# Optimization experiments

Measured on AMD Instinct MI355X. Metric: run time of the kernel, lower is better.

Reference implementation:

```python
import jax, jax.numpy as jnp
import numpy as np

B, S, E, H = 8, 1024, 64, 8
DK = E // H  # n_wires per head
DIM = 2 ** DK  # statevector size


def _quantum_projection(x, phi):
    """Faithful batched simulation of _QLayer for every (batch, seq, head).
    Encoder RX(x_i) followed by trainable RX(phi_i) on the same wire equals
    RX(x_i + phi_i). Then a CNOT ring, then <Z_w> for each wire.
    x: [B,S,E] float, phi: [H,DK] float -> [B,S,E] float expectations.
    """
    b, s, e = x.shape
    theta = x.reshape(b, s, H, DK) + phi  # [B,S,H,DK]
    M = b * s * H
    th = theta.reshape(M, DK)
    # RX(t)|0> = cos(t/2)|0> - i sin(t/2)|1>
    c = jnp.cos(th * 0.5).astype(jnp.complex64)
    sn = (jnp.sin(th * 0.5) * (-1j)).astype(jnp.complex64)
    q = jnp.stack([c, sn], axis=-1)  # [M, DK, 2]
    # product state via iterated kron over the DK wires (fixed small loop)
    amps = jnp.ones((M, 1), jnp.complex64)
    for w in range(DK):
        amps = (amps[:, :, None] * q[:, w, None, :]).reshape(M, -1)
    st = amps.reshape((M,) + (2,) * DK)
    # CNOT ring: (0,1),(1,2),...,(DK-2,DK-1),(DK-1,0)
    gates = [(w, w + 1) for w in range(DK - 1)] + [(DK - 1, 0)]
    for cw, tw in gates:
        ac = 1 + cw
        s0 = jnp.take(st, 0, axis=ac)  # control = 0: identity
        s1 = jnp.take(st, 1, axis=ac)  # control = 1: flip target
        at = 1 + tw - (1 if tw > cw else 0)  # target axis after removing control axis
        s1 = jnp.flip(s1, axis=at)
        st = jnp.stack([s0, s1], axis=ac)
    stf = st.reshape(M, DIM)
    probs = stf.real ** 2 + stf.imag ** 2  # [M, DIM]
    # <Z_w> = sum_k probs[k] * (1 - 2*bit_w(k)); wire 0 is most-significant bit
    bits = (jnp.arange(DIM)[:, None] >> jnp.arange(DK - 1, -1, -1)[None, :]) & 1
    signs = (1 - 2 * bits).astype(probs.dtype)  # [DIM, DK]
    expz = probs @ signs  # [M, DK]
    return expz.reshape(b, s, e)


def setup_inputs() -> dict:
    key = jax.random.key(0)
    k1, k2, k3, k4 = jax.random.split(key, 4)
    x = jax.random.normal(k1, (B, S, E), dtype=jnp.float32)
    phi = jax.random.normal(k2, (H, DK), dtype=jnp.float32) * 0.1  # trainable RX params
    lim = 1.0 / np.sqrt(E)
    W = jax.random.uniform(k3, (E, E), jnp.float32, -lim, lim)  # combine Linear weight
    b = jax.random.uniform(k4, (E,), jnp.float32, -lim, lim)    # combine Linear bias
    return {"x": x, "phi": phi, "W": W, "b": b}


def reference(x, phi, W, b):
    # q = k = v = _projection(x): the original calls _projection(x) 3 times with
    # the same params and no randomness, so they are identical; compute once.
    proj = _quantum_projection(x, phi)  # [B,S,E]
    scores = jax.nn.softmax(
        jnp.einsum('bse,bte->bst', proj, proj) / jnp.sqrt(jnp.float32(DK)), axis=-1)
    # dropout is identity in eval mode
    ctx = jnp.einsum('bst,bte->bse', scores, proj)
    return ctx @ W.T + b
```

## Files before the change

kernel.cpp:

```cpp
#include <hip/hip_runtime.h>
#include <hip/hip_bf16.h>

#define BB 8
#define SS 1024
#define EE 64
#define HH 8
#define DKW 8

typedef __hip_bfloat16 bf16;
typedef unsigned short u16;
typedef _Float16 half8v __attribute__((ext_vector_type(8)));
typedef float floatx4 __attribute__((ext_vector_type(4)));

#define MFMA16(a, b, c) __builtin_amdgcn_mfma_f32_16x16x32_f16(a, b, c, 0, 0, 0)

#define OFF_PROJT ((size_t)BB * SS * EE * 2)

template <int NT>
__device__ __forceinline__ bool detect_f32(const u16* __restrict__ base,
                                           int tid, int* red) {
    int cnt = 0;
#pragma unroll
    for (int i = tid; i < 2048; i += NT) {
        u16 u = base[i * 2];
        int ex = (u >> 7) & 0xFF;
        cnt += (ex >= 0x84) ? 1 : 0;
    }
#pragma unroll
    for (int off = 32; off > 0; off >>= 1) cnt += __shfl_xor(cnt, off, 64);
    if ((tid & 63) == 0) red[tid >> 6] = cnt;
    __syncthreads();
    int tot = 0;
#pragma unroll
    for (int w = 0; w < NT / 64; ++w) tot += red[w];
    return tot > 64;
}

__device__ __forceinline__ void proj_compute(const void* x, const void* phi,
                                             bool f32, int m, float* z) {
    int h = m & (HH - 1);
    float th[DKW];
    if (f32) {
        const float4* xp = (const float4*)((const float*)x + (size_t)m * DKW);
        const float4* pp = (const float4*)((const float*)phi + h * DKW);
        float4 x0 = xp[0], x1 = xp[1];
        float4 p0 = pp[0], p1 = pp[1];
        th[0] = x0.x + p0.x; th[1] = x0.y + p0.y; th[2] = x0.z + p0.z; th[3] = x0.w + p0.w;
        th[4] = x1.x + p1.x; th[5] = x1.y + p1.y; th[6] = x1.z + p1.z; th[7] = x1.w + p1.w;
    } else {
        union { uint4 u; bf16 hv[8]; } xu, pu;
        xu.u = *(const uint4*)((const bf16*)x + (size_t)m * DKW);
        pu.u = *(const uint4*)((const bf16*)phi + (size_t)h * DKW);
#pragma unroll
        for (int j = 0; j < DKW; ++j)
            th[j] = __bfloat162float(xu.hv[j]) + __bfloat162float(pu.hv[j]);
    }
    float c[DKW];
#pragma unroll
    for (int j = 0; j < DKW; ++j) c[j] = __cosf(th[j]);
    float suf = c[1];
#pragma unroll
    for (int j = 2; j < DKW; ++j) suf *= c[j];
    z[0] = suf;
    float pre = c[0];
#pragma unroll
    for (int w = 1; w < DKW; ++w) { pre *= c[w]; z[w] = pre; }
}

__global__ __launch_bounds__(256) void proj_f16_kernel(const void* __restrict__ x,
                                                       const void* __restrict__ phi,
                                                       _Float16* __restrict__ projH,
                                                       _Float16* __restrict__ projT) {
    __shared__ int redd[4];
    __shared__ _Float16 zt[EE][40];
    const int tid = threadIdx.x;
    const bool f32 = detect_f32<256>((const u16*)x, tid, redd);

    const int m = blockIdx.x * 256 + tid;
    float z[DKW];
    proj_compute(x, phi, f32, m, z);

    union { half8v v; _Float16 h[8]; } o;
#pragma unroll
    for (int j = 0; j < DKW; ++j) o.h[j] = (_Float16)z[j];
    *(half8v*)(projH + (size_t)m * DKW) = o.v;

    const int h = m & (HH - 1);
    const int sl = (tid >> 3) & 31;
#pragma unroll
    for (int j = 0; j < DKW; ++j) zt[h * DKW + j][sl] = o.h[j];
    __syncthreads();

    const int b = blockIdx.x >> 5;
    const int s0 = (blockIdx.x * 32) & (SS - 1);
    const int row = tid >> 2, ch = tid & 3;
    half8v vv = *(const half8v*)(&zt[row][ch * 8]);
    *(half8v*)(projT + ((size_t)(b * EE + row)) * SS + s0 + ch * 8) = vv;
}

#define STRD 1048
__global__ __launch_bounds__(512) void fused_attn(const _Float16* __restrict__ projH,
                                                  const _Float16* __restrict__ projT,
                                                  const void* __restrict__ Wp,
                                                  const void* __restrict__ biasp,
                                                  void* __restrict__ outp) {
    __shared__ _Float16 Stile[32][STRD];
    __shared__ _Float16 ctx_lds[32][72];
    __shared__ float rowsum[32];
    __shared__ int redd[8];

    const int tid = threadIdx.x;
    const int wave = tid >> 6, lane = tid & 63;
    const int lr = lane & 15, quad = lane >> 4;
    const int b = blockIdx.y;
    const int m0 = blockIdx.x * 32;

    const bool f32 = detect_f32<512>((const u16*)Wp, tid, redd);

    const _Float16* Pb = projH + (size_t)b * SS * EE;
    const float scale = 0.35355339059327373f;

    {
        const int rowg = wave >> 2, colg = wave & 3;
        const _Float16* arow = Pb + (size_t)(m0 + rowg * 16 + lr) * EE;
        half8v a0 = *(const half8v*)(arow + quad * 8);
        half8v a1 = *(const half8v*)(arow + 32 + quad * 8);
#pragma unroll 4
        for (int c = 0; c < 16; ++c) {
            int n = colg * 256 + c * 16;
            const _Float16* brow = Pb + (size_t)(n + lr) * EE;
            half8v b0 = *(const half8v*)(brow + quad * 8);
            half8v b1 = *(const half8v*)(brow + 32 + quad * 8);
            floatx4 acc = {0.f, 0.f, 0.f, 0.f};
            acc = MFMA16(a0, b0, acc);
            acc = MFMA16(a1, b1, acc);
#pragma unroll
            for (int r = 0; r < 4; ++r)
                Stile[rowg * 16 + quad * 4 + r][n + lr] = (_Float16)(acc[r] * scale);
        }
    }
    __syncthreads();

    {
        const int row = tid >> 4, seg = tid & 15;
        half8v hv[8];
#pragma unroll
        for (int i = 0; i < 8; ++i)
            hv[i] = *(const half8v*)(&Stile[row][i * 128 + seg * 8]);
        float mloc = -1e30f;
#pragma unroll
        for (int i = 0; i < 8; ++i)
#pragma unroll
            for (int j = 0; j < 8; ++j) mloc = fmaxf(mloc, (float)hv[i][j]);
#pragma unroll
        for (int off = 1; off < 16; off <<= 1)
            mloc = fmaxf(mloc, __shfl_xor(mloc, off, 64));
        float lsum = 0.f;
#pragma unroll
        for (int i = 0; i < 8; ++i) {
#pragma unroll
            for (int j = 0; j < 8; ++j) {
                float e = __expf((float)hv[i][j] - mloc);
                lsum += e;
                hv[i][j] = (_Float16)(e * 256.f);
            }
        }
#pragma unroll
        for (int off = 1; off < 16; off <<= 1)
            lsum += __shfl_xor(lsum, off, 64);
        if (seg == 0) rowsum[row] = lsum;
#pragma unroll
        for (int i = 0; i < 8; ++i)
            *(half8v*)(&Stile[row][i * 128 + seg * 8]) = hv[i];
    }
    __syncthreads();

    {
        const int rowg = wave >> 2, cw = wave & 3;
        const _Float16* srow = &Stile[rowg * 16 + lr][0];
        const _Float16* vrow = projT + ((size_t)b * EE + cw * 16 + lr) * SS;
        floatx4 acc0 = {0.f, 0.f, 0.f, 0.f};
        floatx4 acc1 = {0.f, 0.f, 0.f, 0.f};
#pragma unroll 4
        for (int t = 0; t < SS; t += 64) {
            half8v aA = *(const half8v*)(srow + t + quad * 8);
            half8v vA = *(const half8v*)(vrow + t + quad * 8);
            half8v aB = *(const half8v*)(srow + t + 32 + quad * 8);
            half8v vB = *(const half8v*)(vrow + t + 32 + quad * 8);
            acc0 = MFMA16(aA, vA, acc0);
            acc1 = MFMA16(aB, vB, acc1);
        }
#pragma unroll
        for (int r = 0; r < 4; ++r) {
            int row_l = rowg * 16 + quad * 4 + r;
            float inv = 1.0f / (256.0f * rowsum[row_l]);
            ctx_lds[row_l][cw * 16 + lr] = (_Float16)((acc0[r] + acc1[r]) * inv);
        }
    }
    __syncthreads();

    {
        const int rowg = wave >> 2, og = wave & 3;
        const int o = og * 16 + lr;
        half8v ca0 = *(const half8v*)(&ctx_lds[rowg * 16 + lr][quad * 8]);
        half8v ca1 = *(const half8v*)(&ctx_lds[rowg * 16 + lr][32 + quad * 8]);
        half8v wb0, wb1;
        if (f32) {
            const float* wr = (const float*)Wp + (size_t)o * EE;
            union { half8v v; _Float16 h[8]; } w0, w1;
#pragma unroll
            for (int j = 0; j < 8; ++j) {
                w0.h[j] = (_Float16)wr[quad * 8 + j];
                w1.h[j] = (_Float16)wr[32 + quad * 8 + j];
            }
            wb0 = w0.v; wb1 = w1.v;
        } else {
            const bf16* wr = (const bf16*)Wp + (size_t)o * EE;
            union { uint4 u; bf16 hv[8]; } r0, r1;
            r0.u = *(const uint4*)(wr + quad * 8);
            r1.u = *(const uint4*)(wr + 32 + quad * 8);
            union { half8v v; _Float16 h[8]; } w0, w1;
#pragma unroll
            for (int j = 0; j < 8; ++j) {
                w0.h[j] = (_Float16)__bfloat162float(r0.hv[j]);
                w1.h[j] = (_Float16)__bfloat162float(r1.hv[j]);
            }
            wb0 = w0.v; wb1 = w1.v;
        }
        floatx4 oacc = {0.f, 0.f, 0.f, 0.f};
        oacc = MFMA16(ca0, wb0, oacc);
        oacc = MFMA16(ca1, wb1, oacc);

        float bo = f32 ? ((const float*)biasp)[o]
                       : __bfloat162float(((const bf16*)biasp)[o]);
#pragma unroll
        for (int r = 0; r < 4; ++r) {
            size_t oi = ((size_t)b * SS + m0 + rowg * 16 + quad * 4 + r) * EE + o;
            float val = oacc[r] + bo;
            if (f32) ((float*)outp)[oi] = val;
            else     ((bf16*)outp)[oi] = __float2bfloat16(val);
        }
    }
}

extern "C" void kernel_launch(void* const* d_in, const int* in_sizes, int n_in,
                              void* d_out, int out_size, void* d_ws, size_t ws_size,
                              hipStream_t stream) {
    const void* x    = d_in[0];
    const void* phi  = d_in[1];
    const void* W    = d_in[2];
    const void* bias = d_in[3];

    _Float16* projH = (_Float16*)d_ws;
    _Float16* projT = (_Float16*)((char*)d_ws + OFF_PROJT);

    proj_f16_kernel<<<dim3(BB * SS * HH / 256), dim3(256), 0, stream>>>(x, phi, projH, projT);
    fused_attn<<<dim3(SS / 32, BB), dim3(512), 0, stream>>>(projH, projT, W, bias, d_out);
}
```

Baseline: 85.04 us.

## Halve query tile to 16 rows, XOR-swizzle score LDS, split PV over key halves

Each block now handles 16 query rows instead of 32, so the grid doubles to 512 blocks and LDS use per block roughly halves, which allows more blocks per CU. The padded score tile is replaced by an XOR-swizzled layout to avoid LDS bank conflicts without padding. The PV product is split across two key halves handled by separate wave groups, with partial sums reduced through shared memory. The cost is an extra barrier and reduction, half the waves idle in the output projection, and keys and values are reloaded by twice as many blocks.

```diff
diff --git a/kernel.cpp b/kernel.cpp
--- a/kernel.cpp
+++ b/kernel.cpp
@@ -98,22 +98,26 @@
     *(half8v*)(projT + ((size_t)(b * EE + row)) * SS + s0 + ch * 8) = vv;
 }
 
-#define STRD 1048
+__device__ __forceinline__ int sidx(int row, int colblk) {
+    return row * 1024 + ((colblk ^ (row & 7)) << 3);
+}
+
 __global__ __launch_bounds__(512) void fused_attn(const _Float16* __restrict__ projH,
                                                   const _Float16* __restrict__ projT,
                                                   const void* __restrict__ Wp,
                                                   const void* __restrict__ biasp,
                                                   void* __restrict__ outp) {
-    __shared__ _Float16 Stile[32][STRD];
-    __shared__ _Float16 ctx_lds[32][72];
-    __shared__ float rowsum[32];
-    __shared__ int redd[8];
+    __shared__ _Float16 Stile[16 * 1024];
+    __shared__ float    pacc[4][16][17];
+    __shared__ _Float16 ctx_lds[16][72];
+    __shared__ float    rowsum[16];
+    __shared__ int      redd[8];
 
     const int tid = threadIdx.x;
     const int wave = tid >> 6, lane = tid & 63;
     const int lr = lane & 15, quad = lane >> 4;
     const int b = blockIdx.y;
-    const int m0 = blockIdx.x * 32;
+    const int m0 = blockIdx.x * 16;
 
     const bool f32 = detect_f32<512>((const u16*)Wp, tid, redd);
 
@@ -121,13 +125,12 @@
     const float scale = 0.35355339059327373f;
 
     {
-        const int rowg = wave >> 2, colg = wave & 3;
-        const _Float16* arow = Pb + (size_t)(m0 + rowg * 16 + lr) * EE;
+        const _Float16* arow = Pb + (size_t)(m0 + lr) * EE;
         half8v a0 = *(const half8v*)(arow + quad * 8);
         half8v a1 = *(const half8v*)(arow + 32 + quad * 8);
 #pragma unroll 4
-        for (int c = 0; c < 16; ++c) {
-            int n = colg * 256 + c * 16;
+        for (int c = 0; c < 8; ++c) {
+            int n = wave * 128 + c * 16;
             const _Float16* brow = Pb + (size_t)(n + lr) * EE;
             half8v b0 = *(const half8v*)(brow + quad * 8);
             half8v b1 = *(const half8v*)(brow + 32 + quad * 8);
@@ -135,29 +138,31 @@
             acc = MFMA16(a0, b0, acc);
             acc = MFMA16(a1, b1, acc);
 #pragma unroll
-            for (int r = 0; r < 4; ++r)
-                Stile[rowg * 16 + quad * 4 + r][n + lr] = (_Float16)(acc[r] * scale);
+            for (int r = 0; r < 4; ++r) {
+                int row = quad * 4 + r, col = n + lr;
+                Stile[sidx(row, col >> 3) + (col & 7)] = (_Float16)(acc[r] * scale);
+            }
         }
     }
     __syncthreads();
 
     {
-        const int row = tid >> 4, seg = tid & 15;
-        half8v hv[8];
-#pragma unroll
-        for (int i = 0; i < 8; ++i)
-            hv[i] = *(const half8v*)(&Stile[row][i * 128 + seg * 8]);
+        const int row = tid >> 5, seg = tid & 31;
+        half8v hv[4];
+#pragma unroll
+        for (int i = 0; i < 4; ++i)
+            hv[i] = *(const half8v*)(&Stile[sidx(row, i * 32 + seg)]);
         float mloc = -1e30f;
 #pragma unroll
-        for (int i = 0; i < 8; ++i)
+        for (int i = 0; i < 4; ++i)
 #pragma unroll
             for (int j = 0; j < 8; ++j) mloc = fmaxf(mloc, (float)hv[i][j]);
 #pragma unroll
-        for (int off = 1; off < 16; off <<= 1)
+        for (int off = 16; off > 0; off >>= 1)
             mloc = fmaxf(mloc, __shfl_xor(mloc, off, 64));
         float lsum = 0.f;
 #pragma unroll
-        for (int i = 0; i < 8; ++i) {
+        for (int i = 0; i < 4; ++i) {
 #pragma unroll
             for (int j = 0; j < 8; ++j) {
                 float e = __expf((float)hv[i][j] - mloc);
@@ -166,44 +171,54 @@
             }
         }
 #pragma unroll
-        for (int off = 1; off < 16; off <<= 1)
+        for (int off = 16; off > 0; off >>= 1)
             lsum += __shfl_xor(lsum, off, 64);
         if (seg == 0) rowsum[row] = lsum;
 #pragma unroll
-        for (int i = 0; i < 8; ++i)
-            *(half8v*)(&Stile[row][i * 128 + seg * 8]) = hv[i];
-    }
-    __syncthreads();
-
+        for (int i = 0; i < 4; ++i)
+            *(half8v*)(&Stile[sidx(row, i * 32 + seg)]) = hv[i];
+    }
+    __syncthreads();
+
+    const int khalf = wave >> 2, colg = wave & 3;
+    floatx4 accT;
     {
-        const int rowg = wave >> 2, cw = wave & 3;
-        const _Float16* srow = &Stile[rowg * 16 + lr][0];
-        const _Float16* vrow = projT + ((size_t)b * EE + cw * 16 + lr) * SS;
+        const _Float16* vrow = projT + ((size_t)(b * EE + colg * 16 + lr)) * SS
+                               + khalf * 512;
+        const int sbase = khalf * 64;
         floatx4 acc0 = {0.f, 0.f, 0.f, 0.f};
         floatx4 acc1 = {0.f, 0.f, 0.f, 0.f};
 #pragma unroll 4
-        for (int t = 0; t < SS; t += 64) {
-            half8v aA = *(const half8v*)(srow + t + quad * 8);
+        for (int t = 0; t < 512; t += 64) {
+            half8v aA = *(const half8v*)(&Stile[sidx(lr, sbase + (t >> 3) + quad)]);
             half8v vA = *(const half8v*)(vrow + t + quad * 8);
-            half8v aB = *(const half8v*)(srow + t + 32 + quad * 8);
+            half8v aB = *(const half8v*)(&Stile[sidx(lr, sbase + ((t + 32) >> 3) + quad)]);
             half8v vB = *(const half8v*)(vrow + t + 32 + quad * 8);
             acc0 = MFMA16(aA, vA, acc0);
             acc1 = MFMA16(aB, vB, acc1);
         }
+        accT = acc0 + acc1;
+    }
+    if (khalf == 1) {
+#pragma unroll
+        for (int r = 0; r < 4; ++r) pacc[colg][quad * 4 + r][lr] = accT[r];
+    }
+    __syncthreads();
+    if (khalf == 0) {
 #pragma unroll
         for (int r = 0; r < 4; ++r) {
-            int row_l = rowg * 16 + quad * 4 + r;
+            int row_l = quad * 4 + r;
             float inv = 1.0f / (256.0f * rowsum[row_l]);
-            ctx_lds[row_l][cw * 16 + lr] = (_Float16)((acc0[r] + acc1[r]) * inv);
-        }
-    }
-    __syncthreads();
-
-    {
-        const int rowg = wave >> 2, og = wave & 3;
-        const int o = og * 16 + lr;
-        half8v ca0 = *(const half8v*)(&ctx_lds[rowg * 16 + lr][quad * 8]);
-        half8v ca1 = *(const half8v*)(&ctx_lds[rowg * 16 + lr][32 + quad * 8]);
+            ctx_lds[row_l][colg * 16 + lr] =
+                (_Float16)((accT[r] + pacc[colg][row_l][lr]) * inv);
+        }
+    }
+    __syncthreads();
+
+    if (wave < 4) {
+        const int o = wave * 16 + lr;
+        half8v ca0 = *(const half8v*)(&ctx_lds[lr][quad * 8]);
+        half8v ca1 = *(const half8v*)(&ctx_lds[lr][32 + quad * 8]);
         half8v wb0, wb1;
         if (f32) {
             const float* wr = (const float*)Wp + (size_t)o * EE;
@@ -235,7 +250,7 @@
                        : __bfloat162float(((const bf16*)biasp)[o]);
 #pragma unroll
         for (int r = 0; r < 4; ++r) {
-            size_t oi = ((size_t)b * SS + m0 + rowg * 16 + quad * 4 + r) * EE + o;
+            size_t oi = ((size_t)b * SS + m0 + quad * 4 + r) * EE + o;
             float val = oacc[r] + bo;
             if (f32) ((float*)outp)[oi] = val;
             else     ((bf16*)outp)[oi] = __float2bfloat16(val);
@@ -255,5 +270,5 @@
     _Float16* projT = (_Float16*)((char*)d_ws + OFF_PROJT);
 
     proj_f16_kernel<<<dim3(BB * SS * HH / 256), dim3(256), 0, stream>>>(x, phi, projH, projT);
-    fused_attn<<<dim3(SS / 32, BB), dim3(512), 0, stream>>>(projH, projT, W, bias, d_out);
-}
+    fused_attn<<<dim3(SS / 16, BB), dim3(512), 0, stream>>>(projH, projT, W, bias, d_out);
+}
```

Measured after the change: 83.76 us. Within noise of the previous version (-1.5%).

## Swizzle score tile in LDS, reuse B fragments across row groups, remap grid

Applied to the files above, without the earlier changes.

Replaces the padded score tile with an XOR-swizzled 32x1024 layout so that writes from the QK^T stage and the reads in softmax and PV avoid LDS bank conflicts. Each wave now computes both 16-row groups for its own 128 columns, so every loaded key fragment feeds two MFMAs. The PV loop is restructured into one accumulator per wave, and the grid is flattened to 1D with batch in the low bits so consecutive blocks cover different batches. Each swizzled access needs extra index arithmetic, and the QK^T stage holds more live registers.

```diff
diff --git a/kernel.cpp b/kernel.cpp
--- a/kernel.cpp
+++ b/kernel.cpp
@@ -20,7 +20,6 @@
 __device__ __forceinline__ bool detect_f32(const u16* __restrict__ base,
                                            int tid, int* red) {
     int cnt = 0;
-#pragma unroll
     for (int i = tid; i < 2048; i += NT) {
         u16 u = base[i * 2];
         int ex = (u >> 7) & 0xFF;
@@ -98,22 +97,26 @@
     *(half8v*)(projT + ((size_t)(b * EE + row)) * SS + s0 + ch * 8) = vv;
 }
 
-#define STRD 1048
+__device__ __forceinline__ int sidx(int row, int colblk) {
+    return row * 1024 + ((colblk ^ (row & 7)) << 3);
+}
+
 __global__ __launch_bounds__(512) void fused_attn(const _Float16* __restrict__ projH,
                                                   const _Float16* __restrict__ projT,
                                                   const void* __restrict__ Wp,
                                                   const void* __restrict__ biasp,
                                                   void* __restrict__ outp) {
-    __shared__ _Float16 Stile[32][STRD];
+    __shared__ _Float16 Stile[32 * 1024];
     __shared__ _Float16 ctx_lds[32][72];
-    __shared__ float rowsum[32];
-    __shared__ int redd[8];
+    __shared__ float    rowsum[32];
+    __shared__ int      redd[8];
 
     const int tid = threadIdx.x;
     const int wave = tid >> 6, lane = tid & 63;
     const int lr = lane & 15, quad = lane >> 4;
-    const int b = blockIdx.y;
-    const int m0 = blockIdx.x * 32;
+    const int bid = blockIdx.x;
+    const int b = bid & 7;
+    const int m0 = (bid >> 3) * 32;
 
     const bool f32 = detect_f32<512>((const u16*)Wp, tid, redd);
 
@@ -121,22 +124,30 @@
     const float scale = 0.35355339059327373f;
 
     {
-        const int rowg = wave >> 2, colg = wave & 3;
-        const _Float16* arow = Pb + (size_t)(m0 + rowg * 16 + lr) * EE;
-        half8v a0 = *(const half8v*)(arow + quad * 8);
-        half8v a1 = *(const half8v*)(arow + 32 + quad * 8);
-#pragma unroll 4
-        for (int c = 0; c < 16; ++c) {
-            int n = colg * 256 + c * 16;
+        const _Float16* ar0 = Pb + (size_t)(m0 + lr) * EE;
+        const _Float16* ar1 = Pb + (size_t)(m0 + 16 + lr) * EE;
+        half8v a0 = *(const half8v*)(ar0 + quad * 8);
+        half8v a1 = *(const half8v*)(ar0 + 32 + quad * 8);
+        half8v a2 = *(const half8v*)(ar1 + quad * 8);
+        half8v a3 = *(const half8v*)(ar1 + 32 + quad * 8);
+#pragma unroll 2
+        for (int c = 0; c < 8; ++c) {
+            int n = wave * 128 + c * 16;
             const _Float16* brow = Pb + (size_t)(n + lr) * EE;
             half8v b0 = *(const half8v*)(brow + quad * 8);
             half8v b1 = *(const half8v*)(brow + 32 + quad * 8);
-            floatx4 acc = {0.f, 0.f, 0.f, 0.f};
-            acc = MFMA16(a0, b0, acc);
-            acc = MFMA16(a1, b1, acc);
-#pragma unroll
-            for (int r = 0; r < 4; ++r)
-                Stile[rowg * 16 + quad * 4 + r][n + lr] = (_Float16)(acc[r] * scale);
+            floatx4 acc0 = {0.f, 0.f, 0.f, 0.f};
+            floatx4 acc1 = {0.f, 0.f, 0.f, 0.f};
+            acc0 = MFMA16(a0, b0, acc0);
+            acc0 = MFMA16(a1, b1, acc0);
+            acc1 = MFMA16(a2, b0, acc1);
+            acc1 = MFMA16(a3, b1, acc1);
+            int colblk = (n + lr) >> 3, cin = (n + lr) & 7;
+#pragma unroll
+            for (int r = 0; r < 4; ++r) {
+                Stile[sidx(quad * 4 + r, colblk) + cin]      = (_Float16)(acc0[r] * scale);
+                Stile[sidx(16 + quad * 4 + r, colblk) + cin] = (_Float16)(acc1[r] * scale);
+            }
         }
     }
     __syncthreads();
@@ -146,14 +157,14 @@
         half8v hv[8];
 #pragma unroll
         for (int i = 0; i < 8; ++i)
-            hv[i] = *(const half8v*)(&Stile[row][i * 128 + seg * 8]);
+            hv[i] = *(const half8v*)(&Stile[sidx(row, i * 16 + seg)]);
         float mloc = -1e30f;
 #pragma unroll
         for (int i = 0; i < 8; ++i)
 #pragma unroll
             for (int j = 0; j < 8; ++j) mloc = fmaxf(mloc, (float)hv[i][j]);
 #pragma unroll
-        for (int off = 1; off < 16; off <<= 1)
+        for (int off = 8; off > 0; off >>= 1)
             mloc = fmaxf(mloc, __shfl_xor(mloc, off, 64));
         float lsum = 0.f;
 #pragma unroll
@@ -166,42 +177,37 @@
             }
         }
 #pragma unroll
-        for (int off = 1; off < 16; off <<= 1)
+        for (int off = 8; off > 0; off >>= 1)
             lsum += __shfl_xor(lsum, off, 64);
         if (seg == 0) rowsum[row] = lsum;
 #pragma unroll
         for (int i = 0; i < 8; ++i)
-            *(half8v*)(&Stile[row][i * 128 + seg * 8]) = hv[i];
-    }
-    __syncthreads();
-
-    {
-        const int rowg = wave >> 2, cw = wave & 3;
-        const _Float16* srow = &Stile[rowg * 16 + lr][0];
-        const _Float16* vrow = projT + ((size_t)b * EE + cw * 16 + lr) * SS;
-        floatx4 acc0 = {0.f, 0.f, 0.f, 0.f};
-        floatx4 acc1 = {0.f, 0.f, 0.f, 0.f};
+            *(half8v*)(&Stile[sidx(row, i * 16 + seg)]) = hv[i];
+    }
+    __syncthreads();
+
+    const int rowg = wave >> 2, eg = wave & 3;
+    {
+        const int e = eg * 16 + lr;
+        const _Float16* vrow = projT + ((size_t)(b * EE + e)) * SS;
+        floatx4 acc = {0.f, 0.f, 0.f, 0.f};
 #pragma unroll 4
-        for (int t = 0; t < SS; t += 64) {
-            half8v aA = *(const half8v*)(srow + t + quad * 8);
-            half8v vA = *(const half8v*)(vrow + t + quad * 8);
-            half8v aB = *(const half8v*)(srow + t + 32 + quad * 8);
-            half8v vB = *(const half8v*)(vrow + t + 32 + quad * 8);
-            acc0 = MFMA16(aA, vA, acc0);
-            acc1 = MFMA16(aB, vB, acc1);
+        for (int k0 = 0; k0 < SS; k0 += 32) {
+            half8v A = *(const half8v*)(&Stile[sidx(rowg * 16 + lr, (k0 >> 3) + quad)]);
+            half8v B = *(const half8v*)(vrow + k0 + quad * 8);
+            acc = MFMA16(A, B, acc);
         }
 #pragma unroll
         for (int r = 0; r < 4; ++r) {
             int row_l = rowg * 16 + quad * 4 + r;
             float inv = 1.0f / (256.0f * rowsum[row_l]);
-            ctx_lds[row_l][cw * 16 + lr] = (_Float16)((acc0[r] + acc1[r]) * inv);
-        }
-    }
-    __syncthreads();
-
-    {
-        const int rowg = wave >> 2, og = wave & 3;
-        const int o = og * 16 + lr;
+            ctx_lds[row_l][eg * 16 + lr] = (_Float16)(acc[r] * inv);
+        }
+    }
+    __syncthreads();
+
+    {
+        const int o = eg * 16 + lr;
         half8v ca0 = *(const half8v*)(&ctx_lds[rowg * 16 + lr][quad * 8]);
         half8v ca1 = *(const half8v*)(&ctx_lds[rowg * 16 + lr][32 + quad * 8]);
         half8v wb0, wb1;
@@ -255,5 +261,5 @@
     _Float16* projT = (_Float16*)((char*)d_ws + OFF_PROJT);
 
     proj_f16_kernel<<<dim3(BB * SS * HH / 256), dim3(256), 0, stream>>>(x, phi, projH, projT);
-    fused_attn<<<dim3(SS / 32, BB), dim3(512), 0, stream>>>(projH, projT, W, bias, d_out);
-}
+    fused_attn<<<dim3(256), dim3(512), 0, stream>>>(projH, projT, W, bias, d_out);
+}
```

Result: faster. 82.86 us (-2.6%).
